# Kernel tuning notes

Hardware: AMD Instinct MI355X
Metric: run time of the kernel (lower is better)

## Reference

```python
import jax, jax.numpy as jnp
import numpy as np

SPHERE_RADIUS = 1.0
DISTANCE_ERROR = 0.002
BIG = 1e10  # sentinel for 'no intersection'


def setup_inputs() -> dict:
    key = jax.random.key(0)
    k1, k2 = jax.random.split(key)
    x = jax.random.normal(k1, (1, 1048576, 7), dtype=jnp.float32)
    z = jax.random.normal(k2, (1, 384), dtype=jnp.float32)
    return {"x": x, "z": z}


def reference(x, z):
    # x: [B, N, 7] = origin(3), time(1), direction(3)
    # z: [B, 6*S]  = per-sphere center(3), velocity(3)
    B, N, _ = x.shape
    origin = x[..., 0:3]                      # [B, N, 3]
    t_ray = x[..., 3:4]                       # [B, N, 1] ray time
    direction = x[..., 4:7]                   # [B, N, 3]
    d = direction / (jnp.linalg.norm(direction, axis=-1, keepdims=True) + 1e-12)

    spheres = z.reshape(B, -1, 6)             # [B, S, 6]
    sph_c = spheres[..., 0:3]                 # [B, S, 3]
    sph_v = spheres[..., 3:6]                 # [B, S, 3]

    # play sphere forward to ray time: center(t) = c + v * t  -> [B, N, S, 3]
    center_t = sph_c[:, None, :, :] + sph_v[:, None, :, :] * t_ray[..., None]

    oc = center_t - origin[:, :, None, :]     # [B, N, S, 3]
    b = jnp.einsum('bnd,bnsd->bns', d, oc)    # projection of oc on ray dir
    c = jnp.einsum('bnsd,bnsd->bns', oc, oc) - SPHERE_RADIUS * SPHERE_RADIUS
    disc = b * b - c                          # [B, N, S]

    sq = jnp.sqrt(jnp.where(disc > 0, disc, 1.0))  # safe sqrt
    t0 = b - sq
    t1 = b + sq
    t_hit = jnp.where(t0 > 0, t0, t1)         # nearest non-negative root
    valid = (disc >= 0) & (t1 > 0)
    dist = jnp.where(valid, t_hit, BIG)       # [B, N, S]

    closest = jnp.min(dist, axis=-1)          # min-distance reduction over spheres
    mu = closest.reshape(1, N, 1)
    sigma = jnp.full((1, N, 1), DISTANCE_ERROR, dtype=x.dtype)
    return mu, sigma
```

## Files before the change

### kernel.cpp

```cpp
#include <hip/hip_runtime.h>


typedef float v2f __attribute__((ext_vector_type(2)));

constexpr int NSPH = 64;
constexpr float BIGF = 1e10f;

__global__ __launch_bounds__(256, 8) void ray_sphere_kernel(
    const float* __restrict__ x, const float* __restrict__ z,
    float* __restrict__ out, int N)
{
    int pair = blockIdx.x * 256 + threadIdx.x;
    int n0 = pair * 2;
    if (n0 >= N) return;

    const float* xr = x + (long)n0 * 7;
    v2f ox = {xr[0], xr[7]};
    v2f oy = {xr[1], xr[8]};
    v2f oz = {xr[2], xr[9]};
    v2f t  = {xr[3], xr[10]};
    v2f dx = {xr[4], xr[11]};
    v2f dy = {xr[5], xr[12]};
    v2f dz = {xr[6], xr[13]};

    v2f n2 = __builtin_elementwise_fma(dx, dx,
             __builtin_elementwise_fma(dy, dy, dz * dz));
    v2f inv;
    inv[0] = __builtin_amdgcn_rcpf(__builtin_amdgcn_sqrtf(n2[0]) + 1e-12f);
    inv[1] = __builtin_amdgcn_rcpf(__builtin_amdgcn_sqrtf(n2[1]) + 1e-12f);
    dx *= inv; dy *= inv; dz *= inv;

    v2f closest = {BIGF, BIGF};

    #pragma unroll 16
    for (int s = 0; s < NSPH; ++s) {
        const float* zs = z + s * 6;
        float cx = zs[0], cy = zs[1], cz = zs[2];
        float vx = zs[3], vy = zs[4], vz = zs[5];

        v2f ocx = __builtin_elementwise_fma((v2f){vx, vx}, t, cx - ox);
        v2f ocy = __builtin_elementwise_fma((v2f){vy, vy}, t, cy - oy);
        v2f ocz = __builtin_elementwise_fma((v2f){vz, vz}, t, cz - oz);

        v2f b = __builtin_elementwise_fma(dx, ocx,
                __builtin_elementwise_fma(dy, ocy, dz * ocz));
        v2f csq = __builtin_elementwise_fma(ocx, ocx,
                  __builtin_elementwise_fma(ocy, ocy, ocz * ocz));
        v2f disc = __builtin_elementwise_fma(b, b, 1.0f - csq);

        v2f sq;
        sq[0] = __builtin_amdgcn_sqrtf(disc[0]);
        sq[1] = __builtin_amdgcn_sqrtf(disc[1]);

        v2f t0 = b - sq;
        v2f t1 = b + sq;

        #pragma unroll
        for (int k = 0; k < 2; ++k) {
            float r1 = (t1[k] > 0.0f) ? t1[k] : BIGF;
            float r  = (t0[k] > 0.0f) ? t0[k] : r1;
            closest[k] = fminf(closest[k], r);
        }
    }

    *(v2f*)(out + n0) = closest;
    *(v2f*)(out + N + n0) = (v2f){0.002f, 0.002f};
}

extern "C" void kernel_launch(void* const* d_in, const int* in_sizes, int n_in,
                              void* d_out, int out_size, void* d_ws, size_t ws_size,
                              hipStream_t stream) {
    const float* x = (const float*)d_in[0];
    const float* z = (const float*)d_in[1];
    float* out = (float*)d_out;
    int N = in_sizes[0] / 7;

    int pairs = N / 2;
    int blocks = (pairs + 255) / 256;
    ray_sphere_kernel<<<blocks, 256, 0, stream>>>(x, z, out, N);
}
```

Baseline: 34.61 us.

## Process four rays per thread with float4 vectorized input loads

Each thread now handles four rays instead of two. It loads the 28 contiguous input floats as seven float4 loads and unpacks them into two packed-float pairs. Each sphere's parameters are loaded once and reused across four rays, which amortizes the scalar z loads and loop overhead, and the outputs are written with float4 stores. This raises per-thread register use and halves the thread count, which may reduce latency hiding. It also assumes N is a multiple of 4 and that the input is 16-byte aligned.

Result: no change. 34.89 us (+0.8%).

```diff
diff --git a/kernel.cpp b/kernel.cpp
--- a/kernel.cpp
+++ b/kernel.cpp
@@ -6,65 +6,92 @@
 constexpr int NSPH = 64;
 constexpr float BIGF = 1e10f;
 
+__device__ __forceinline__ void step2(
+    const v2f& ox, const v2f& oy, const v2f& oz, const v2f& t,
+    const v2f& dx, const v2f& dy, const v2f& dz,
+    float cx, float cy, float cz, float vx, float vy, float vz,
+    v2f& closest)
+{
+    v2f ocx = __builtin_elementwise_fma((v2f){vx, vx}, t, cx - ox);
+    v2f ocy = __builtin_elementwise_fma((v2f){vy, vy}, t, cy - oy);
+    v2f ocz = __builtin_elementwise_fma((v2f){vz, vz}, t, cz - oz);
+    v2f b = __builtin_elementwise_fma(dx, ocx,
+            __builtin_elementwise_fma(dy, ocy, dz * ocz));
+    v2f csq = __builtin_elementwise_fma(ocx, ocx,
+              __builtin_elementwise_fma(ocy, ocy, ocz * ocz));
+    v2f disc = __builtin_elementwise_fma(b, b, (v2f){1.0f, 1.0f} - csq);
+
+    v2f sq;
+    sq[0] = __builtin_amdgcn_sqrtf(disc[0]);
+    sq[1] = __builtin_amdgcn_sqrtf(disc[1]);
+
+    v2f t0 = b - sq;
+    v2f t1 = b + sq;
+
+    #pragma unroll
+    for (int k = 0; k < 2; ++k) {
+        float r1 = (t1[k] > 0.0f) ? t1[k] : BIGF;
+        float r  = (t0[k] > 0.0f) ? t0[k] : r1;
+        closest[k] = fminf(closest[k], r);
+    }
+}
+
 __global__ __launch_bounds__(256, 8) void ray_sphere_kernel(
     const float* __restrict__ x, const float* __restrict__ z,
     float* __restrict__ out, int N)
 {
-    int pair = blockIdx.x * 256 + threadIdx.x;
-    int n0 = pair * 2;
+    int tid = blockIdx.x * 256 + threadIdx.x;
+    long n0 = (long)tid * 4;
     if (n0 >= N) return;
 
-    const float* xr = x + (long)n0 * 7;
-    v2f ox = {xr[0], xr[7]};
-    v2f oy = {xr[1], xr[8]};
-    v2f oz = {xr[2], xr[9]};
-    v2f t  = {xr[3], xr[10]};
-    v2f dx = {xr[4], xr[11]};
-    v2f dy = {xr[5], xr[12]};
-    v2f dz = {xr[6], xr[13]};
+    const float4* xr = (const float4*)(x + n0 * 7);
+    float4 w0 = xr[0], w1 = xr[1], w2 = xr[2], w3 = xr[3],
+           w4 = xr[4], w5 = xr[5], w6 = xr[6];
 
-    v2f n2 = __builtin_elementwise_fma(dx, dx,
-             __builtin_elementwise_fma(dy, dy, dz * dz));
-    v2f inv;
-    inv[0] = __builtin_amdgcn_rcpf(__builtin_amdgcn_sqrtf(n2[0]) + 1e-12f);
-    inv[1] = __builtin_amdgcn_rcpf(__builtin_amdgcn_sqrtf(n2[1]) + 1e-12f);
-    dx *= inv; dy *= inv; dz *= inv;
+    v2f oxA = {w0.x, w1.w}, oyA = {w0.y, w2.x}, ozA = {w0.z, w2.y};
+    v2f tA  = {w0.w, w2.z};
+    v2f dxA = {w1.x, w2.w}, dyA = {w1.y, w3.x}, dzA = {w1.z, w3.y};
 
-    v2f closest = {BIGF, BIGF};
+    v2f oxB = {w3.z, w5.y}, oyB = {w3.w, w5.z}, ozB = {w4.x, w5.w};
+    v2f tB  = {w4.y, w6.x};
+    v2f dxB = {w4.z, w6.y}, dyB = {w4.w, w6.z}, dzB = {w5.x, w6.w};
 
-    #pragma unroll 16
+    {
+        v2f n2 = __builtin_elementwise_fma(dxA, dxA,
+                 __builtin_elementwise_fma(dyA, dyA, dzA * dzA));
+        v2f inv;
+        inv[0] = __builtin_amdgcn_rcpf(__builtin_amdgcn_sqrtf(n2[0]) + 1e-12f);
+        inv[1] = __builtin_amdgcn_rcpf(__builtin_amdgcn_sqrtf(n2[1]) + 1e-12f);
+        dxA *= inv; dyA *= inv; dzA *= inv;
+    }
+    {
+        v2f n2 = __builtin_elementwise_fma(dxB, dxB,
+                 __builtin_elementwise_fma(dyB, dyB, dzB * dzB));
+        v2f inv;
+        inv[0] = __builtin_amdgcn_rcpf(__builtin_amdgcn_sqrtf(n2[0]) + 1e-12f);
+        inv[1] = __builtin_amdgcn_rcpf(__builtin_amdgcn_sqrtf(n2[1]) + 1e-12f);
+        dxB *= inv; dyB *= inv; dzB *= inv;
+    }
+
+    v2f closestA = {BIGF, BIGF};
+    v2f closestB = {BIGF, BIGF};
+
+    #pragma unroll 8
     for (int s = 0; s < NSPH; ++s) {
         const float* zs = z + s * 6;
         float cx = zs[0], cy = zs[1], cz = zs[2];
         float vx = zs[3], vy = zs[4], vz = zs[5];
-
-        v2f ocx = __builtin_elementwise_fma((v2f){vx, vx}, t, cx - ox);
-        v2f ocy = __builtin_elementwise_fma((v2f){vy, vy}, t, cy - oy);
-        v2f ocz = __builtin_elementwise_fma((v2f){vz, vz}, t, cz - oz);
-
-        v2f b = __builtin_elementwise_fma(dx, ocx,
-                __builtin_elementwise_fma(dy, ocy, dz * ocz));
-        v2f csq = __builtin_elementwise_fma(ocx, ocx,
-                  __builtin_elementwise_fma(ocy, ocy, ocz * ocz));
-        v2f disc = __builtin_elementwise_fma(b, b, 1.0f - csq);
-
-        v2f sq;
-        sq[0] = __builtin_amdgcn_sqrtf(disc[0]);
-        sq[1] = __builtin_amdgcn_sqrtf(disc[1]);
-
-        v2f t0 = b - sq;
-        v2f t1 = b + sq;
-
-        #pragma unroll
-        for (int k = 0; k < 2; ++k) {
-            float r1 = (t1[k] > 0.0f) ? t1[k] : BIGF;
-            float r  = (t0[k] > 0.0f) ? t0[k] : r1;
-            closest[k] = fminf(closest[k], r);
-        }
+        step2(oxA, oyA, ozA, tA, dxA, dyA, dzA, cx, cy, cz, vx, vy, vz, closestA);
+        step2(oxB, oyB, ozB, tB, dxB, dyB, dzB, cx, cy, cz, vx, vy, vz, closestB);
     }
 
-    *(v2f*)(out + n0) = closest;
-    *(v2f*)(out + N + n0) = (v2f){0.002f, 0.002f};
+    float4 mu;
+    mu.x = closestA[0];
+    mu.y = closestA[1];
+    mu.z = closestB[0];
+    mu.w = closestB[1];
+    *(float4*)(out + n0) = mu;
+    *(float4*)(out + N + n0) = make_float4(0.002f, 0.002f, 0.002f, 0.002f);
 }
 
 extern "C" void kernel_launch(void* const* d_in, const int* in_sizes, int n_in,
@@ -75,7 +102,7 @@
     float* out = (float*)d_out;
     int N = in_sizes[0] / 7;
 
-    int pairs = N / 2;
-    int blocks = (pairs + 255) / 256;
+    int threads = N / 4;
+    int blocks = (threads + 255) / 256;
     ray_sphere_kernel<<<blocks, 256, 0, stream>>>(x, z, out, N);
 }
```
